# Optimization experiments

Hardware: AMD Instinct MI355X
Metric: run time of the kernel (lower is better)

## Reference

```python
import jax, jax.numpy as jnp
import numpy as np

N_NODES = 512
STATE_DIM = 32
MESSAGE_DIM = 32
H_MSG = 64
H_RO = 64
N_STEPS = 5


def setup_inputs() -> dict:
    key = jax.random.key(0)
    ks = jax.random.split(key, 20)
    s = 0.01  # torch init: normal(0, 0.01) weights, zero biases
    d, m = STATE_DIM, MESSAGE_DIM
    inp = {
        "J": jax.random.normal(ks[0], (N_NODES, N_NODES), jnp.float32),
        "b": jax.random.normal(ks[1], (N_NODES,), jnp.float32),
        # message-passing MLP
        "mp_W1": jax.random.normal(ks[2], (H_MSG, 2 * d + 3), jnp.float32) * s,
        "mp_b1": jnp.zeros((H_MSG,), jnp.float32),
        "mp_W2": jax.random.normal(ks[3], (H_MSG, H_MSG), jnp.float32) * s,
        "mp_b2": jnp.zeros((H_MSG,), jnp.float32),
        "mp_W3": jax.random.normal(ks[4], (m, H_MSG), jnp.float32) * s,
        "mp_b3": jnp.zeros((m,), jnp.float32),
        # GRU (input = state_dim + message_dim, hidden = state_dim); gate order r,z,n
        "gru_Wih": jax.random.normal(ks[5], (3 * d, d + m), jnp.float32) * 0.1,
        "gru_Whh": jax.random.normal(ks[6], (3 * d, d), jnp.float32) * 0.1,
        "gru_bih": jax.random.normal(ks[7], (3 * d,), jnp.float32) * 0.1,
        "gru_bhh": jax.random.normal(ks[8], (3 * d,), jnp.float32) * 0.1,
        # readout MLP
        "r_W1": jax.random.normal(ks[9], (H_RO, d), jnp.float32) * s,
        "r_b1": jnp.zeros((H_RO,), jnp.float32),
        "r_W2": jax.random.normal(ks[10], (H_RO, H_RO), jnp.float32) * s,
        "r_b2": jnp.zeros((H_RO,), jnp.float32),
        "r_W3": jax.random.normal(ks[11], (2, H_RO), jnp.float32) * s,
        "r_b3": jnp.zeros((2,), jnp.float32),
    }
    return inp


def reference(J, b, mp_W1, mp_b1, mp_W2, mp_b2, mp_W3, mp_b3,
              gru_Wih, gru_Whh, gru_bih, gru_bhh,
              r_W1, r_b1, r_W2, r_b2, r_W3, r_b3):
    n = J.shape[0]
    d = gru_Whh.shape[1]
    # split first message-layer weight by input segments to avoid building [n,n,2d+3]
    Wi, Wj = mp_W1[:, :d], mp_W1[:, d:2 * d]          # [H, d]
    wJ, wbi, wbj = mp_W1[:, 2 * d], mp_W1[:, 2 * d + 1], mp_W1[:, 2 * d + 2]  # [H]

    def step(h, _):
        # pre[i, j, :] = W1 @ cat(h_i, h_j, J_ij, b_i, b_j) + b1
        pre = ((h @ Wi.T)[:, None, :] + (h @ Wj.T)[None, :, :]
               + J[:, :, None] * wJ + b[:, None, None] * wbi
               + b[None, :, None] * wbj + mp_b1)          # [n, n, H]
        m1 = jax.nn.relu(pre)
        m2 = jax.nn.relu(m1 @ mp_W2.T + mp_b2)            # [n, n, H]
        msg = jax.nn.relu(m2 @ mp_W3.T + mp_b3)           # [n, n, M]
        msg_sum = msg.sum(axis=0)                         # sum over senders i -> [n, M]
        # GRU cell over all nodes (torch GRU, gate order r,z,n)
        x = jnp.concatenate([h, msg_sum], axis=-1)        # [n, d+M]
        gi = x @ gru_Wih.T + gru_bih                      # [n, 3d]
        gh = h @ gru_Whh.T + gru_bhh                      # [n, 3d]
        i_r, i_z, i_n = jnp.split(gi, 3, axis=-1)
        h_r, h_z, h_n = jnp.split(gh, 3, axis=-1)
        r = jax.nn.sigmoid(i_r + h_r)
        z = jax.nn.sigmoid(i_z + h_z)
        n_g = jnp.tanh(i_n + r * h_n)
        h_new = (1.0 - z) * n_g + z * h
        return h_new, None

    h0 = jnp.zeros((n, d), J.dtype)
    h, _ = jax.lax.scan(step, h0, None, length=N_STEPS)
    y = jax.nn.relu(h @ r_W1.T + r_b1)
    y = jax.nn.relu(y @ r_W2.T + r_b2)
    y = jax.nn.relu(y @ r_W3.T + r_b3)                    # [n, 2]
    return jax.nn.sigmoid(y)
```

## Files before the change

kernel.cpp:

```cpp
#include <hip/hip_runtime.h>
#include <math.h>

#define NN 512
#define SD 32
#define HM 64

typedef _Float16 f16x8 __attribute__((ext_vector_type(8)));
typedef float floatx4 __attribute__((ext_vector_type(4)));
typedef unsigned uintx4 __attribute__((ext_vector_type(4)));

#define OFF_HBS   0
#define OFF_M2L   73728
#define OFF_MSUM  92160
#define OFF_HPREV 93184
#define OFF_HS    93440
#define OFF_MSG   93696
#define OFF_GI    93952
#define OFF_GH    94720
#define LDS_TOTAL 95488

__device__ __forceinline__ float sigmoidf_(float x) {
    return 1.0f / (1.0f + __expf(-x));
}
__device__ __forceinline__ unsigned pkrtz(float a, float b) {
    unsigned r;
    asm("v_cvt_pkrtz_f16_f32 %0, %1, %2" : "=v"(r) : "v"(a), "v"(b));
    return r;
}
__device__ __forceinline__ unsigned pk_add(unsigned a, unsigned b) {
    unsigned r;
    asm("v_pk_add_f16 %0, %1, %2" : "=v"(r) : "v"(a), "v"(b));
    return r;
}
__device__ __forceinline__ unsigned pk_fma(unsigned a, unsigned b, unsigned c) {
    unsigned r;
    asm("v_pk_fma_f16 %0, %1, %2, %3" : "=v"(r) : "v"(a), "v"(b), "v"(c));
    return r;
}
__device__ __forceinline__ unsigned pk_relu(unsigned a) {
    unsigned r, z = 0u;
    asm("v_pk_max_f16 %0, %1, %2" : "=v"(r) : "v"(a), "v"(z));
    return r;
}

struct PParams {
    const float *J, *b, *mpW1, *mpb1, *mpW2, *mpW3, *Wih, *Whh, *rW1, *rW2;
    float *JT, *W1T, *WihT, *WhhT, *rW1T, *rW2T;
    unsigned *w2p, *w3p, *wjp, *hb0, *hjp0;
};

__global__ __launch_bounds__(256) void prep_kernel(PParams pp)
{
    __shared__ float tile[32][33];
    const int tid = threadIdx.x;
    const int b   = blockIdx.x;
    {
        int bx = b & 15, by = b >> 4;
        int tx = tid & 31, ty = tid >> 5;
        #pragma unroll
        for (int r = 0; r < 32; r += 8)
            tile[ty + r][tx] = pp.J[(by * 32 + ty + r) * NN + bx * 32 + tx];
        __syncthreads();
        #pragma unroll
        for (int r = 0; r < 32; r += 8)
            pp.JT[(bx * 32 + ty + r) * NN + by * 32 + tx] = tile[tx][ty + r];
    }
    if (b == 0 && tid < 64) {
        int l = tid, qq = l >> 4, cc = l & 15;
        for (int f = 0; f < 2; ++f)
            for (int t4 = 0; t4 < 4; ++t4) {
                const float* src = pp.mpW2 + (t4 * 16 + cc) * 64 + f * 32 + qq * 8;
                unsigned* dst = pp.w2p + ((f * 4 + t4) * 64 + l) * 4;
                for (int i = 0; i < 4; ++i) dst[i] = pkrtz(src[2 * i], src[2 * i + 1]);
            }
        for (int f = 0; f < 2; ++f)
            for (int t2 = 0; t2 < 2; ++t2) {
                const float* src = pp.mpW3 + (t2 * 16 + cc) * 64 + f * 32 + qq * 8;
                unsigned* dst = pp.w3p + ((f * 2 + t2) * 64 + l) * 4;
                for (int i = 0; i < 4; ++i) dst[i] = pkrtz(src[2 * i], src[2 * i + 1]);
            }
        for (int s = 0; s < 2; ++s) {
            unsigned* dst = pp.wjp + (s * 64 + l) * 4;
            for (int i = 0; i < 4; ++i) {
                int r0 = qq * 8 + 2 * i + s * 32;
                dst[i] = pkrtz(pp.mpW1[r0 * 67 + 64], pp.mpW1[(r0 + 1) * 67 + 64]);
            }
        }
    }
    if (b == 1)
        for (int n = tid; n < 64 * 67; n += 256) {
            int cc = n / 67, d = n % 67;
            pp.W1T[d * 64 + cc] = pp.mpW1[n];
        }
    if (b == 2)
        for (int n = tid; n < 96 * 64; n += 256)
            pp.WihT[(n & 63) * 96 + (n >> 6)] = pp.Wih[n];
    if (b == 3)
        for (int n = tid; n < 96 * 32; n += 256)
            pp.WhhT[(n & 31) * 96 + (n >> 5)] = pp.Whh[n];
    if (b == 4) {
        for (int n = tid; n < 64 * 32; n += 256)
            pp.rW1T[(n & 31) * 64 + (n >> 5)] = pp.rW1[n];
        for (int n = tid; n < 64 * 64; n += 256)
            pp.rW2T[(n & 63) * 64 + (n >> 6)] = pp.rW2[n];
    }
    if (b >= 16 && b < 144) {
        int jj = (b - 16) * 4 + (tid >> 6);
        int cc = tid & 63;
        float bj = pp.b[jj];
        float sj = bj * pp.mpW1[cc * 67 + 66] + pp.mpb1[cc];
        float si = bj * pp.mpW1[cc * 67 + 65];
        float sjp = __shfl(sj, cc ^ 1);
        float sip = __shfl(si, cc ^ 1);
        if (!(cc & 1)) {
            pp.hjp0[jj * 32 + (cc >> 1)] = pkrtz(sj, sjp);
            pp.hb0[jj * 32 + (cc >> 1)]  = pkrtz(si, sip);
        }
    }
}

struct SParams {
    const unsigned *hbR;  unsigned *hbW;
    const unsigned *hjR;  unsigned *hjW;
    const float *hR;      float *hW;
    const float *JT, *W1T, *WihT, *WhhT, *bih, *bhh, *mpb2, *mpb3, *b, *mpb1;
    const float *rW1T, *rW2T, *rW3, *rb1, *rb2, *rb3;
    const unsigned *w2p, *w3p, *wjp;
    float *out;
    int hzero, rdout;
};

__global__ __launch_bounds__(512, 1) void step_kernel(SParams s)
{
    extern __shared__ __align__(16) char smem[];
    char* hbS = smem + OFF_HBS;
    float (*msum)[32]   = (float(*)[32])(smem + OFF_MSUM);
    float (*hPrevS)[32] = (float(*)[32])(smem + OFF_HPREV);
    float (*hS)[32]     = (float(*)[32])(smem + OFF_HS);
    float (*msgS)[32]   = (float(*)[32])(smem + OFF_MSG);
    float (*giS)[96]    = (float(*)[96])(smem + OFF_GI);
    float (*ghS)[96]    = (float(*)[96])(smem + OFF_GH);

    const int tid  = threadIdx.x;
    const int lane = tid & 63;
    const int wave = tid >> 6;
    const int nsel = wave >> 2;
    const int nw   = wave & 3;
    const int j    = blockIdx.x * 2 + nsel;
    const int q    = lane >> 4;
    const int c    = lane & 15;
    char* m2Lw = smem + OFF_M2L + wave * 2304;

    {
        uintx4 cr[8];
        const uintx4* gp = (const uintx4*)s.hbR;
        #pragma unroll
        for (int k = 0; k < 8; ++k) cr[k] = gp[k * 512 + tid];
        #pragma unroll
        for (int k = 0; k < 8; ++k) {
            int row = k * 64 + (tid >> 3);
            *(uintx4*)(hbS + row * 144 + (tid & 7) * 16) = cr[k];
        }
    }
    if (tid < 64 && !s.hzero)
        hPrevS[tid >> 5][tid & 31] = s.hR[blockIdx.x * 64 + tid];
    __syncthreads();

    f16x8 Aw2[2][4], Aw3[2][2];
    #pragma unroll
    for (int f = 0; f < 2; ++f)
        #pragma unroll
        for (int t4 = 0; t4 < 4; ++t4)
            Aw2[f][t4] = __builtin_bit_cast(f16x8,
                ((const uintx4*)s.w2p)[(f * 4 + t4) * 64 + lane]);
    #pragma unroll
    for (int f = 0; f < 2; ++f)
        #pragma unroll
        for (int t2 = 0; t2 < 2; ++t2)
            Aw3[f][t2] = __builtin_bit_cast(f16x8,
                ((const uintx4*)s.w3p)[(f * 2 + t2) * 64 + lane]);
    uintx4 wja = ((const uintx4*)s.wjp)[lane];
    uintx4 wjb = ((const uintx4*)s.wjp)[64 + lane];
    uintx4 hja = ((const uintx4*)s.hjR)[j * 8 + q];
    uintx4 hjb = ((const uintx4*)s.hjR)[j * 8 + 4 + q];

    floatx4 b2i[4], b3i[2];
    #pragma unroll
    for (int t4 = 0; t4 < 4; ++t4)
        #pragma unroll
        for (int r = 0; r < 4; ++r) b2i[t4][r] = s.mpb2[t4 * 16 + q * 4 + r];
    #pragma unroll
    for (int t2 = 0; t2 < 2; ++t2)
        #pragma unroll
        for (int r = 0; r < 4; ++r) b3i[t2][r] = s.mpb3[t2 * 16 + q * 4 + r];

    const float jA = s.JT[j * NN + (8 * q + nw) * 16 + c];
    const float jB = s.JT[j * NN + (8 * q + 4 + nw) * 16 + c];

    float accf[2][4];
    #pragma unroll
    for (int t2 = 0; t2 < 2; ++t2)
        #pragma unroll
        for (int r = 0; r < 4; ++r) accf[t2][r] = 0.0f;

    auto edge_group = [&](int G, float Jv) {
        const char* rb = hbS + (G * 16 + c) * 144;
        uintx4 vlo = *(const uintx4*)(rb + q * 16);
        uintx4 vhi = *(const uintx4*)(rb + 64 + q * 16);
        const unsigned Jp = pkrtz(Jv, Jv);

        uintx4 a0u, a1u;
        #pragma unroll
        for (int i = 0; i < 4; ++i) {
            a0u[i] = pk_relu(pk_fma(Jp, wja[i], pk_add(vlo[i], hja[i])));
            a1u[i] = pk_relu(pk_fma(Jp, wjb[i], pk_add(vhi[i], hjb[i])));
        }
        f16x8 B0 = __builtin_bit_cast(f16x8, a0u);
        f16x8 B1 = __builtin_bit_cast(f16x8, a1u);

        floatx4 c1[4];
        #pragma unroll
        for (int t4 = 0; t4 < 4; ++t4) {
            c1[t4] = __builtin_amdgcn_mfma_f32_16x16x32_f16(Aw2[0][t4], B0, b2i[t4], 0, 0, 0);
            c1[t4] = __builtin_amdgcn_mfma_f32_16x16x32_f16(Aw2[1][t4], B1, c1[t4], 0, 0, 0);
        }
        #pragma unroll
        for (int t4 = 0; t4 < 4; ++t4) {
            unsigned p0 = pkrtz(fmaxf(c1[t4][0], 0.f), fmaxf(c1[t4][1], 0.f));
            unsigned p1 = pkrtz(fmaxf(c1[t4][2], 0.f), fmaxf(c1[t4][3], 0.f));
            *(uint2*)(m2Lw + c * 144 + t4 * 32 + q * 8) = make_uint2(p0, p1);
        }
        uintx4 rlo = *(const uintx4*)(m2Lw + c * 144 + q * 16);
        uintx4 rhi = *(const uintx4*)(m2Lw + c * 144 + 64 + q * 16);
        f16x8 B2lo = __builtin_bit_cast(f16x8, rlo);
        f16x8 B2hi = __builtin_bit_cast(f16x8, rhi);

        floatx4 c2[2];
        #pragma unroll
        for (int t2 = 0; t2 < 2; ++t2) {
            c2[t2] = __builtin_amdgcn_mfma_f32_16x16x32_f16(Aw3[0][t2], B2lo, b3i[t2], 0, 0, 0);
            c2[t2] = __builtin_amdgcn_mfma_f32_16x16x32_f16(Aw3[1][t2], B2hi, c2[t2], 0, 0, 0);
        }
        #pragma unroll
        for (int t2 = 0; t2 < 2; ++t2)
            #pragma unroll
            for (int r = 0; r < 4; ++r)
                accf[t2][r] += fmaxf(c2[t2][r], 0.0f);
    };

    #pragma unroll
    for (int k = 0; k < 4; ++k) {
        edge_group(8 * k + nw,     __shfl(jA, k * 16 + c));
        edge_group(8 * k + 4 + nw, __shfl(jB, k * 16 + c));
    }

    #pragma unroll
    for (int m = 1; m < 16; m <<= 1)
        #pragma unroll
        for (int t2 = 0; t2 < 2; ++t2)
            #pragma unroll
            for (int r = 0; r < 4; ++r)
                accf[t2][r] += __shfl_xor(accf[t2][r], m);
    if (c == 0) {
        #pragma unroll
        for (int t2 = 0; t2 < 2; ++t2)
            #pragma unroll
            for (int r = 0; r < 4; ++r)
                msum[wave][t2 * 16 + q * 4 + r] = accf[t2][r];
    }
    __syncthreads();

    if (tid < 64) {
        int node = tid >> 5, d = tid & 31;
        msgS[node][d] = msum[node * 4 + 0][d] + msum[node * 4 + 1][d] +
                        msum[node * 4 + 2][d] + msum[node * 4 + 3][d];
    }
    __syncthreads();

    if (tid < 192) {
        int node = tid / 96, r = tid % 96;
        float a  = s.bih[r];
        float bb = s.bhh[r];
        if (!s.hzero) {
            #pragma unroll
            for (int k = 0; k < 32; ++k) {
                float hv = hPrevS[node][k];
                a  = fmaf(hv, s.WihT[k * 96 + r], a);
                bb = fmaf(hv, s.WhhT[k * 96 + r], bb);
            }
        }
        #pragma unroll
        for (int k = 0; k < 32; ++k)
            a = fmaf(msgS[node][k], s.WihT[(32 + k) * 96 + r], a);
        giS[node][r] = a; ghS[node][r] = bb;
    }
    __syncthreads();

    if (tid < 64) {
        int node = tid >> 5, d = tid & 31;
        float r  = sigmoidf_(giS[node][d] + ghS[node][d]);
        float z  = sigmoidf_(giS[node][32 + d] + ghS[node][32 + d]);
        float ng = tanhf(giS[node][64 + d] + r * ghS[node][64 + d]);
        float hold = s.hzero ? 0.0f : hPrevS[node][d];
        float hv = (1.0f - z) * ng + z * hold;
        hS[node][d] = hv;
        s.hW[blockIdx.x * 64 + tid] = hv;
    }
    __syncthreads();

    if (!s.rdout) {
        if (tid < 128) {
            int node = tid >> 6, cc = tid & 63;
            int jj = blockIdx.x * 2 + node;
            float bj = s.b[jj];
            float si = bj * s.W1T[65 * 64 + cc];
            float sj = bj * s.W1T[66 * 64 + cc] + s.mpb1[cc];
            #pragma unroll
            for (int d = 0; d < 32; ++d) {
                float hv = hS[node][d];
                si = fmaf(hv, s.W1T[d * 64 + cc], si);
                sj = fmaf(hv, s.W1T[(32 + d) * 64 + cc], sj);
            }
            float sip = __shfl(si, lane ^ 1);
            float sjp = __shfl(sj, lane ^ 1);
            if (!(cc & 1)) {
                s.hbW[jj * 32 + (cc >> 1)] = pkrtz(si, sip);
                s.hjW[jj * 32 + (cc >> 1)] = pkrtz(sj, sjp);
            }
        }
    } else {
        if (wave < 2) {
            int node = wave;
            int jj = blockIdx.x * 2 + node;
            float y1 = s.rb1[lane];
            #pragma unroll
            for (int k = 0; k < 32; ++k)
                y1 = fmaf(hS[node][k], s.rW1T[k * 64 + lane], y1);
            y1 = fmaxf(y1, 0.0f);
            float y2 = s.rb2[lane];
            #pragma unroll
            for (int k = 0; k < 64; ++k)
                y2 = fmaf(__shfl(y1, k), s.rW2T[k * 64 + lane], y2);
            y2 = fmaxf(y2, 0.0f);
            float y3 = (lane < 2) ? s.rb3[lane] : 0.0f;
            #pragma unroll
            for (int k = 0; k < 64; ++k) {
                float v = __shfl(y2, k);
                if (lane < 2) y3 = fmaf(v, s.rW3[lane * 64 + k], y3);
            }
            if (lane < 2) s.out[jj * 2 + lane] = sigmoidf_(y3);
        }
    }
}

extern "C" void kernel_launch(void* const* d_in, const int* in_sizes, int n_in,
                              void* d_out, int out_size, void* d_ws, size_t ws_size,
                              hipStream_t stream)
{
    float* ws = (float*)d_ws;

    const float* J    = (const float*)d_in[0];
    const float* b    = (const float*)d_in[1];
    const float* mpW1 = (const float*)d_in[2];
    const float* mpb1 = (const float*)d_in[3];
    const float* mpW2 = (const float*)d_in[4];
    const float* mpb2 = (const float*)d_in[5];
    const float* mpW3 = (const float*)d_in[6];
    const float* mpb3 = (const float*)d_in[7];
    const float* Wih  = (const float*)d_in[8];
    const float* Whh  = (const float*)d_in[9];
    const float* bih  = (const float*)d_in[10];
    const float* bhh  = (const float*)d_in[11];
    const float* rW1  = (const float*)d_in[12];
    const float* rb1  = (const float*)d_in[13];
    const float* rW2  = (const float*)d_in[14];
    const float* rb2  = (const float*)d_in[15];
    const float* rW3  = (const float*)d_in[16];
    const float* rb3  = (const float*)d_in[17];

    float*    JT   = ws;
    float*    W1T  = ws + 262144;
    float*    WihT = ws + 266432;
    float*    WhhT = ws + 272576;
    float*    rW1T = ws + 275648;
    float*    rW2T = ws + 277696;
    unsigned* w2p  = (unsigned*)(ws + 281792);
    unsigned* w3p  = (unsigned*)(ws + 283840);
    unsigned* wjp  = (unsigned*)(ws + 284864);
    unsigned* hb0  = (unsigned*)(ws + 285376);
    unsigned* hb1  = (unsigned*)(ws + 301760);
    unsigned* hj0  = (unsigned*)(ws + 318144);
    unsigned* hj1  = (unsigned*)(ws + 334528);
    float*    h0   = ws + 350912;
    float*    h1   = ws + 367296;

    PParams pp;
    pp.J = J; pp.b = b; pp.mpW1 = mpW1; pp.mpb1 = mpb1; pp.mpW2 = mpW2;
    pp.mpW3 = mpW3; pp.Wih = Wih; pp.Whh = Whh; pp.rW1 = rW1; pp.rW2 = rW2;
    pp.JT = JT; pp.W1T = W1T; pp.WihT = WihT; pp.WhhT = WhhT;
    pp.rW1T = rW1T; pp.rW2T = rW2T;
    pp.w2p = w2p; pp.w3p = w3p; pp.wjp = wjp; pp.hb0 = hb0; pp.hjp0 = hj0;

    (void)hipFuncSetAttribute((const void*)step_kernel,
                              hipFuncAttributeMaxDynamicSharedMemorySize, LDS_TOTAL);

    prep_kernel<<<dim3(256), dim3(256), 0, stream>>>(pp);

    SParams s;
    s.JT = JT; s.W1T = W1T; s.WihT = WihT; s.WhhT = WhhT;
    s.bih = bih; s.bhh = bhh; s.mpb2 = mpb2; s.mpb3 = mpb3; s.b = b; s.mpb1 = mpb1;
    s.rW1T = rW1T; s.rW2T = rW2T; s.rW3 = rW3; s.rb1 = rb1; s.rb2 = rb2; s.rb3 = rb3;
    s.w2p = w2p; s.w3p = w3p; s.wjp = wjp;
    s.out = (float*)d_out;

    for (int t = 0; t < 5; ++t) {
        s.hbR = (t & 1) ? hb1 : hb0;
        s.hbW = (t & 1) ? hb0 : hb1;
        s.hjR = (t & 1) ? hj1 : hj0;
        s.hjW = (t & 1) ? hj0 : hj1;
        s.hR  = (t & 1) ? h0 : h1;
        s.hW  = (t & 1) ? h1 : h0;
        s.hzero = (t == 0);
        s.rdout = (t == 4);
        step_kernel<<<dim3(256), dim3(512), LDS_TOTAL, stream>>>(s);
    }
}
```

Measured before the change: 150.7 us.

## Fuse prep and five step launches into one persistent kernel with grid barriers

New measurement: 330.2 us. +119.1%, slower.

```diff
diff --git a/kernel.cpp b/kernel.cpp
--- a/kernel.cpp
+++ b/kernel.cpp
@@ -4,6 +4,7 @@
 #define NN 512
 #define SD 32
 #define HM 64
+#define NB 256
 
 typedef _Float16 f16x8 __attribute__((ext_vector_type(8)));
 typedef float floatx4 __attribute__((ext_vector_type(4)));
@@ -17,7 +18,11 @@
 #define OFF_MSG   93696
 #define OFF_GI    93952
 #define OFF_GH    94720
-#define LDS_TOTAL 95488
+#define OFF_HJ    95488
+#define OFF_W1T   95744
+#define OFF_WIH   113168
+#define OFF_WHH   138000
+#define LDS_TOTAL 150416
 
 __device__ __forceinline__ float sigmoidf_(float x) {
     return 1.0f / (1.0f + __expf(-x));
@@ -43,96 +48,45 @@
     return r;
 }
 
-struct PParams {
-    const float *J, *b, *mpW1, *mpb1, *mpW2, *mpW3, *Wih, *Whh, *rW1, *rW2;
-    float *JT, *W1T, *WihT, *WhhT, *rW1T, *rW2T;
-    unsigned *w2p, *w3p, *wjp, *hb0, *hjp0;
+__device__ __forceinline__ void grid_bar(unsigned long long* pk, unsigned target_gen)
+{
+    __syncthreads();
+    if (threadIdx.x == 0) {
+        unsigned long long old =
+            __hip_atomic_fetch_add(pk, 1ull, __ATOMIC_RELAXED, __HIP_MEMORY_SCOPE_AGENT);
+        if ((unsigned)(old & 0xffffffffull) == (unsigned)(NB - 1))
+            __hip_atomic_store(pk, ((unsigned long long)target_gen) << 32,
+                               __ATOMIC_RELAXED, __HIP_MEMORY_SCOPE_AGENT);
+        while ((unsigned)(__hip_atomic_load(pk, __ATOMIC_RELAXED,
+                                            __HIP_MEMORY_SCOPE_AGENT) >> 32) < target_gen)
+            __builtin_amdgcn_s_sleep(2);
+        (void)__hip_atomic_load(pk, __ATOMIC_ACQUIRE, __HIP_MEMORY_SCOPE_AGENT);
+    }
+    __syncthreads();
+}
+
+struct FParams {
+    const float *J, *b, *mpW1, *mpb1, *mpW2, *mpb2, *mpW3, *mpb3;
+    const float *Wih, *Whh, *bih, *bhh;
+    const float *rW1, *rb1, *rW2, *rb2, *rW3, *rb3;
+    unsigned *hbg;
+    unsigned long long *bar;
+    float *out;
 };
 
-__global__ __launch_bounds__(256) void prep_kernel(PParams pp)
-{
-    __shared__ float tile[32][33];
-    const int tid = threadIdx.x;
-    const int b   = blockIdx.x;
-    {
-        int bx = b & 15, by = b >> 4;
-        int tx = tid & 31, ty = tid >> 5;
-        #pragma unroll
-        for (int r = 0; r < 32; r += 8)
-            tile[ty + r][tx] = pp.J[(by * 32 + ty + r) * NN + bx * 32 + tx];
-        __syncthreads();
-        #pragma unroll
-        for (int r = 0; r < 32; r += 8)
-            pp.JT[(bx * 32 + ty + r) * NN + by * 32 + tx] = tile[tx][ty + r];
-    }
-    if (b == 0 && tid < 64) {
-        int l = tid, qq = l >> 4, cc = l & 15;
-        for (int f = 0; f < 2; ++f)
-            for (int t4 = 0; t4 < 4; ++t4) {
-                const float* src = pp.mpW2 + (t4 * 16 + cc) * 64 + f * 32 + qq * 8;
-                unsigned* dst = pp.w2p + ((f * 4 + t4) * 64 + l) * 4;
-                for (int i = 0; i < 4; ++i) dst[i] = pkrtz(src[2 * i], src[2 * i + 1]);
-            }
-        for (int f = 0; f < 2; ++f)
-            for (int t2 = 0; t2 < 2; ++t2) {
-                const float* src = pp.mpW3 + (t2 * 16 + cc) * 64 + f * 32 + qq * 8;
-                unsigned* dst = pp.w3p + ((f * 2 + t2) * 64 + l) * 4;
-                for (int i = 0; i < 4; ++i) dst[i] = pkrtz(src[2 * i], src[2 * i + 1]);
-            }
-        for (int s = 0; s < 2; ++s) {
-            unsigned* dst = pp.wjp + (s * 64 + l) * 4;
-            for (int i = 0; i < 4; ++i) {
-                int r0 = qq * 8 + 2 * i + s * 32;
-                dst[i] = pkrtz(pp.mpW1[r0 * 67 + 64], pp.mpW1[(r0 + 1) * 67 + 64]);
-            }
-        }
-    }
-    if (b == 1)
-        for (int n = tid; n < 64 * 67; n += 256) {
-            int cc = n / 67, d = n % 67;
-            pp.W1T[d * 64 + cc] = pp.mpW1[n];
-        }
-    if (b == 2)
-        for (int n = tid; n < 96 * 64; n += 256)
-            pp.WihT[(n & 63) * 96 + (n >> 6)] = pp.Wih[n];
-    if (b == 3)
-        for (int n = tid; n < 96 * 32; n += 256)
-            pp.WhhT[(n & 31) * 96 + (n >> 5)] = pp.Whh[n];
-    if (b == 4) {
-        for (int n = tid; n < 64 * 32; n += 256)
-            pp.rW1T[(n & 31) * 64 + (n >> 5)] = pp.rW1[n];
-        for (int n = tid; n < 64 * 64; n += 256)
-            pp.rW2T[(n & 63) * 64 + (n >> 6)] = pp.rW2[n];
-    }
-    if (b >= 16 && b < 144) {
-        int jj = (b - 16) * 4 + (tid >> 6);
-        int cc = tid & 63;
-        float bj = pp.b[jj];
-        float sj = bj * pp.mpW1[cc * 67 + 66] + pp.mpb1[cc];
-        float si = bj * pp.mpW1[cc * 67 + 65];
-        float sjp = __shfl(sj, cc ^ 1);
-        float sip = __shfl(si, cc ^ 1);
-        if (!(cc & 1)) {
-            pp.hjp0[jj * 32 + (cc >> 1)] = pkrtz(sj, sjp);
-            pp.hb0[jj * 32 + (cc >> 1)]  = pkrtz(si, sip);
-        }
-    }
-}
-
-struct SParams {
-    const unsigned *hbR;  unsigned *hbW;
-    const unsigned *hjR;  unsigned *hjW;
-    const float *hR;      float *hW;
-    const float *JT, *W1T, *WihT, *WhhT, *bih, *bhh, *mpb2, *mpb3, *b, *mpb1;
-    const float *rW1T, *rW2T, *rW3, *rb1, *rb2, *rb3;
-    const unsigned *w2p, *w3p, *wjp;
-    float *out;
-    int hzero, rdout;
-};
-
-__global__ __launch_bounds__(512, 1) void step_kernel(SParams s)
+__global__ __launch_bounds__(512, 1) void fused3_kernel(FParams p)
 {
     extern __shared__ __align__(16) char smem[];
+    const int tid  = threadIdx.x;
+    const int bid  = blockIdx.x;
+    const int lane = tid & 63;
+    const int wave = tid >> 6;
+    const int nsel = wave >> 2;
+    const int nw   = wave & 3;
+    const int j    = bid * 2 + nsel;
+    const int q    = lane >> 4;
+    const int c    = lane & 15;
+
     char* hbS = smem + OFF_HBS;
     float (*msum)[32]   = (float(*)[32])(smem + OFF_MSUM);
     float (*hPrevS)[32] = (float(*)[32])(smem + OFF_HPREV);
@@ -140,215 +94,276 @@
     float (*msgS)[32]   = (float(*)[32])(smem + OFF_MSG);
     float (*giS)[96]    = (float(*)[96])(smem + OFF_GI);
     float (*ghS)[96]    = (float(*)[96])(smem + OFF_GH);
-
-    const int tid  = threadIdx.x;
-    const int lane = tid & 63;
-    const int wave = tid >> 6;
-    const int nsel = wave >> 2;
-    const int nw   = wave & 3;
-    const int j    = blockIdx.x * 2 + nsel;
-    const int q    = lane >> 4;
-    const int c    = lane & 15;
-    char* m2Lw = smem + OFF_M2L + wave * 2304;
-
-    {
-        uintx4 cr[8];
-        const uintx4* gp = (const uintx4*)s.hbR;
-        #pragma unroll
-        for (int k = 0; k < 8; ++k) cr[k] = gp[k * 512 + tid];
-        #pragma unroll
-        for (int k = 0; k < 8; ++k) {
-            int row = k * 64 + (tid >> 3);
-            *(uintx4*)(hbS + row * 144 + (tid & 7) * 16) = cr[k];
-        }
+    char*  hjL  = smem + OFF_HJ;
+    float* w1tL = (float*)(smem + OFF_W1T);
+    float* wihL = (float*)(smem + OFF_WIH);
+    float* whhL = (float*)(smem + OFF_WHH);
+    char*  m2Lw = smem + OFF_M2L + wave * 2304;
+
+    for (int n = tid; n < 64 * 67; n += 512) {
+        int cc = n / 67, d = n % 67;
+        w1tL[d * 65 + cc] = p.mpW1[n];
     }
-    if (tid < 64 && !s.hzero)
-        hPrevS[tid >> 5][tid & 31] = s.hR[blockIdx.x * 64 + tid];
-    __syncthreads();
+    for (int n = tid; n < 96 * 64; n += 512)
+        wihL[(n & 63) * 97 + (n >> 6)] = p.Wih[n];
+    for (int n = tid; n < 96 * 32; n += 512)
+        whhL[(n & 31) * 97 + (n >> 5)] = p.Whh[n];
 
     f16x8 Aw2[2][4], Aw3[2][2];
     #pragma unroll
     for (int f = 0; f < 2; ++f)
         #pragma unroll
-        for (int t4 = 0; t4 < 4; ++t4)
-            Aw2[f][t4] = __builtin_bit_cast(f16x8,
-                ((const uintx4*)s.w2p)[(f * 4 + t4) * 64 + lane]);
+        for (int t4 = 0; t4 < 4; ++t4) {
+            const float* src = p.mpW2 + (t4 * 16 + c) * 64 + f * 32 + q * 8;
+            floatx4 s0 = *(const floatx4*)(src);
+            floatx4 s1 = *(const floatx4*)(src + 4);
+            uintx4 u;
+            u[0] = pkrtz(s0[0], s0[1]); u[1] = pkrtz(s0[2], s0[3]);
+            u[2] = pkrtz(s1[0], s1[1]); u[3] = pkrtz(s1[2], s1[3]);
+            Aw2[f][t4] = __builtin_bit_cast(f16x8, u);
+        }
     #pragma unroll
     for (int f = 0; f < 2; ++f)
         #pragma unroll
-        for (int t2 = 0; t2 < 2; ++t2)
-            Aw3[f][t2] = __builtin_bit_cast(f16x8,
-                ((const uintx4*)s.w3p)[(f * 2 + t2) * 64 + lane]);
-    uintx4 wja = ((const uintx4*)s.wjp)[lane];
-    uintx4 wjb = ((const uintx4*)s.wjp)[64 + lane];
-    uintx4 hja = ((const uintx4*)s.hjR)[j * 8 + q];
-    uintx4 hjb = ((const uintx4*)s.hjR)[j * 8 + 4 + q];
-
+        for (int t2 = 0; t2 < 2; ++t2) {
+            const float* src = p.mpW3 + (t2 * 16 + c) * 64 + f * 32 + q * 8;
+            floatx4 s0 = *(const floatx4*)(src);
+            floatx4 s1 = *(const floatx4*)(src + 4);
+            uintx4 u;
+            u[0] = pkrtz(s0[0], s0[1]); u[1] = pkrtz(s0[2], s0[3]);
+            u[2] = pkrtz(s1[0], s1[1]); u[3] = pkrtz(s1[2], s1[3]);
+            Aw3[f][t2] = __builtin_bit_cast(f16x8, u);
+        }
+    uintx4 wja, wjb;
+    #pragma unroll
+    for (int i = 0; i < 4; ++i) {
+        int r0 = q * 8 + 2 * i;
+        wja[i] = pkrtz(p.mpW1[r0 * 67 + 64], p.mpW1[(r0 + 1) * 67 + 64]);
+        int r1 = r0 + 32;
+        wjb[i] = pkrtz(p.mpW1[r1 * 67 + 64], p.mpW1[(r1 + 1) * 67 + 64]);
+    }
     floatx4 b2i[4], b3i[2];
     #pragma unroll
     for (int t4 = 0; t4 < 4; ++t4)
         #pragma unroll
-        for (int r = 0; r < 4; ++r) b2i[t4][r] = s.mpb2[t4 * 16 + q * 4 + r];
+        for (int r = 0; r < 4; ++r) b2i[t4][r] = p.mpb2[t4 * 16 + q * 4 + r];
     #pragma unroll
     for (int t2 = 0; t2 < 2; ++t2)
         #pragma unroll
-        for (int r = 0; r < 4; ++r) b3i[t2][r] = s.mpb3[t2 * 16 + q * 4 + r];
-
-    const float jA = s.JT[j * NN + (8 * q + nw) * 16 + c];
-    const float jB = s.JT[j * NN + (8 * q + 4 + nw) * 16 + c];
-
-    float accf[2][4];
-    #pragma unroll
-    for (int t2 = 0; t2 < 2; ++t2)
-        #pragma unroll
-        for (int r = 0; r < 4; ++r) accf[t2][r] = 0.0f;
-
-    auto edge_group = [&](int G, float Jv) {
-        const char* rb = hbS + (G * 16 + c) * 144;
-        uintx4 vlo = *(const uintx4*)(rb + q * 16);
-        uintx4 vhi = *(const uintx4*)(rb + 64 + q * 16);
-        const unsigned Jp = pkrtz(Jv, Jv);
-
-        uintx4 a0u, a1u;
-        #pragma unroll
-        for (int i = 0; i < 4; ++i) {
-            a0u[i] = pk_relu(pk_fma(Jp, wja[i], pk_add(vlo[i], hja[i])));
-            a1u[i] = pk_relu(pk_fma(Jp, wjb[i], pk_add(vhi[i], hjb[i])));
-        }
-        f16x8 B0 = __builtin_bit_cast(f16x8, a0u);
-        f16x8 B1 = __builtin_bit_cast(f16x8, a1u);
-
-        floatx4 c1[4];
-        #pragma unroll
-        for (int t4 = 0; t4 < 4; ++t4) {
-            c1[t4] = __builtin_amdgcn_mfma_f32_16x16x32_f16(Aw2[0][t4], B0, b2i[t4], 0, 0, 0);
-            c1[t4] = __builtin_amdgcn_mfma_f32_16x16x32_f16(Aw2[1][t4], B1, c1[t4], 0, 0, 0);
-        }
-        #pragma unroll
-        for (int t4 = 0; t4 < 4; ++t4) {
-            unsigned p0 = pkrtz(fmaxf(c1[t4][0], 0.f), fmaxf(c1[t4][1], 0.f));
-            unsigned p1 = pkrtz(fmaxf(c1[t4][2], 0.f), fmaxf(c1[t4][3], 0.f));
-            *(uint2*)(m2Lw + c * 144 + t4 * 32 + q * 8) = make_uint2(p0, p1);
-        }
-        uintx4 rlo = *(const uintx4*)(m2Lw + c * 144 + q * 16);
-        uintx4 rhi = *(const uintx4*)(m2Lw + c * 144 + 64 + q * 16);
-        f16x8 B2lo = __builtin_bit_cast(f16x8, rlo);
-        f16x8 B2hi = __builtin_bit_cast(f16x8, rhi);
-
-        floatx4 c2[2];
-        #pragma unroll
-        for (int t2 = 0; t2 < 2; ++t2) {
-            c2[t2] = __builtin_amdgcn_mfma_f32_16x16x32_f16(Aw3[0][t2], B2lo, b3i[t2], 0, 0, 0);
-            c2[t2] = __builtin_amdgcn_mfma_f32_16x16x32_f16(Aw3[1][t2], B2hi, c2[t2], 0, 0, 0);
-        }
+        for (int r = 0; r < 4; ++r) b3i[t2][r] = p.mpb3[t2 * 16 + q * 4 + r];
+
+    const float jA = p.J[((8 * q + nw) * 16 + c) * NN + j];
+    const float jB = p.J[((8 * q + 4 + nw) * 16 + c) * NN + j];
+
+    __syncthreads();
+
+    if (tid < 128) {
+        int node = tid >> 6, cc = tid & 63;
+        int jj = bid * 2 + node;
+        float bj = p.b[jj];
+        float si = bj * w1tL[65 * 65 + cc];
+        float sj = bj * w1tL[66 * 65 + cc] + p.mpb1[cc];
+        float sip = __shfl(si, lane ^ 1);
+        float sjp = __shfl(sj, lane ^ 1);
+        if (!(cc & 1)) {
+            __hip_atomic_store(&p.hbg[jj * 32 + (cc >> 1)], pkrtz(si, sip),
+                               __ATOMIC_RELAXED, __HIP_MEMORY_SCOPE_AGENT);
+            *(unsigned*)(hjL + node * 128 + (cc >> 1) * 4) = pkrtz(sj, sjp);
+        }
+    }
+    grid_bar(p.bar, 1);
+
+    #pragma unroll 1
+    for (int t = 0; t < 5; ++t) {
+        {
+            const unsigned long long* gq =
+                (const unsigned long long*)(p.hbg + t * 16384);
+            uintx4 cr[8];
+            #pragma unroll
+            for (int k = 0; k < 8; ++k) {
+                unsigned long long lo = __hip_atomic_load(gq + (k * 512 + tid) * 2,
+                    __ATOMIC_RELAXED, __HIP_MEMORY_SCOPE_AGENT);
+                unsigned long long hi = __hip_atomic_load(gq + (k * 512 + tid) * 2 + 1,
+                    __ATOMIC_RELAXED, __HIP_MEMORY_SCOPE_AGENT);
+                cr[k][0] = (unsigned)lo; cr[k][1] = (unsigned)(lo >> 32);
+                cr[k][2] = (unsigned)hi; cr[k][3] = (unsigned)(hi >> 32);
+            }
+            #pragma unroll
+            for (int k = 0; k < 8; ++k) {
+                int row = k * 64 + (tid >> 3);
+                *(uintx4*)(hbS + row * 144 + (tid & 7) * 16) = cr[k];
+            }
+        }
+        uintx4 hja = *(const uintx4*)(hjL + nsel * 128 + q * 16);
+        uintx4 hjb = *(const uintx4*)(hjL + nsel * 128 + 64 + q * 16);
+        __syncthreads();
+
+        float accf[2][4];
         #pragma unroll
         for (int t2 = 0; t2 < 2; ++t2)
             #pragma unroll
-            for (int r = 0; r < 4; ++r)
-                accf[t2][r] += fmaxf(c2[t2][r], 0.0f);
-    };
-
-    #pragma unroll
-    for (int k = 0; k < 4; ++k) {
-        edge_group(8 * k + nw,     __shfl(jA, k * 16 + c));
-        edge_group(8 * k + 4 + nw, __shfl(jB, k * 16 + c));
-    }
-
-    #pragma unroll
-    for (int m = 1; m < 16; m <<= 1)
-        #pragma unroll
-        for (int t2 = 0; t2 < 2; ++t2)
-            #pragma unroll
-            for (int r = 0; r < 4; ++r)
-                accf[t2][r] += __shfl_xor(accf[t2][r], m);
-    if (c == 0) {
-        #pragma unroll
-        for (int t2 = 0; t2 < 2; ++t2)
-            #pragma unroll
-            for (int r = 0; r < 4; ++r)
-                msum[wave][t2 * 16 + q * 4 + r] = accf[t2][r];
-    }
-    __syncthreads();
-
-    if (tid < 64) {
-        int node = tid >> 5, d = tid & 31;
-        msgS[node][d] = msum[node * 4 + 0][d] + msum[node * 4 + 1][d] +
-                        msum[node * 4 + 2][d] + msum[node * 4 + 3][d];
-    }
-    __syncthreads();
-
-    if (tid < 192) {
-        int node = tid / 96, r = tid % 96;
-        float a  = s.bih[r];
-        float bb = s.bhh[r];
-        if (!s.hzero) {
-            #pragma unroll
-            for (int k = 0; k < 32; ++k) {
-                float hv = hPrevS[node][k];
-                a  = fmaf(hv, s.WihT[k * 96 + r], a);
-                bb = fmaf(hv, s.WhhT[k * 96 + r], bb);
-            }
-        }
-        #pragma unroll
-        for (int k = 0; k < 32; ++k)
-            a = fmaf(msgS[node][k], s.WihT[(32 + k) * 96 + r], a);
-        giS[node][r] = a; ghS[node][r] = bb;
-    }
-    __syncthreads();
-
-    if (tid < 64) {
-        int node = tid >> 5, d = tid & 31;
-        float r  = sigmoidf_(giS[node][d] + ghS[node][d]);
-        float z  = sigmoidf_(giS[node][32 + d] + ghS[node][32 + d]);
-        float ng = tanhf(giS[node][64 + d] + r * ghS[node][64 + d]);
-        float hold = s.hzero ? 0.0f : hPrevS[node][d];
-        float hv = (1.0f - z) * ng + z * hold;
-        hS[node][d] = hv;
-        s.hW[blockIdx.x * 64 + tid] = hv;
-    }
-    __syncthreads();
-
-    if (!s.rdout) {
-        if (tid < 128) {
-            int node = tid >> 6, cc = tid & 63;
-            int jj = blockIdx.x * 2 + node;
-            float bj = s.b[jj];
-            float si = bj * s.W1T[65 * 64 + cc];
-            float sj = bj * s.W1T[66 * 64 + cc] + s.mpb1[cc];
-            #pragma unroll
-            for (int d = 0; d < 32; ++d) {
-                float hv = hS[node][d];
-                si = fmaf(hv, s.W1T[d * 64 + cc], si);
-                sj = fmaf(hv, s.W1T[(32 + d) * 64 + cc], sj);
-            }
-            float sip = __shfl(si, lane ^ 1);
-            float sjp = __shfl(sj, lane ^ 1);
-            if (!(cc & 1)) {
-                s.hbW[jj * 32 + (cc >> 1)] = pkrtz(si, sip);
-                s.hjW[jj * 32 + (cc >> 1)] = pkrtz(sj, sjp);
-            }
-        }
-    } else {
-        if (wave < 2) {
-            int node = wave;
-            int jj = blockIdx.x * 2 + node;
-            float y1 = s.rb1[lane];
+            for (int r = 0; r < 4; ++r) accf[t2][r] = 0.0f;
+
+        auto edge_group = [&](int G, float Jv) {
+            const char* rb = hbS + (G * 16 + c) * 144;
+            uintx4 vlo = *(const uintx4*)(rb + q * 16);
+            uintx4 vhi = *(const uintx4*)(rb + 64 + q * 16);
+            const unsigned Jp = pkrtz(Jv, Jv);
+
+            uintx4 a0u, a1u;
+            #pragma unroll
+            for (int i = 0; i < 4; ++i) {
+                a0u[i] = pk_relu(pk_fma(Jp, wja[i], pk_add(vlo[i], hja[i])));
+                a1u[i] = pk_relu(pk_fma(Jp, wjb[i], pk_add(vhi[i], hjb[i])));
+            }
+            f16x8 B0 = __builtin_bit_cast(f16x8, a0u);
+            f16x8 B1 = __builtin_bit_cast(f16x8, a1u);
+
+            floatx4 c1[4];
+            #pragma unroll
+            for (int t4 = 0; t4 < 4; ++t4) {
+                c1[t4] = __builtin_amdgcn_mfma_f32_16x16x32_f16(Aw2[0][t4], B0, b2i[t4], 0, 0, 0);
+                c1[t4] = __builtin_amdgcn_mfma_f32_16x16x32_f16(Aw2[1][t4], B1, c1[t4], 0, 0, 0);
+            }
+            #pragma unroll
+            for (int t4 = 0; t4 < 4; ++t4) {
+                unsigned p0 = pkrtz(fmaxf(c1[t4][0], 0.f), fmaxf(c1[t4][1], 0.f));
+                unsigned p1 = pkrtz(fmaxf(c1[t4][2], 0.f), fmaxf(c1[t4][3], 0.f));
+                *(uint2*)(m2Lw + c * 144 + t4 * 32 + q * 8) = make_uint2(p0, p1);
+            }
+            uintx4 rlo = *(const uintx4*)(m2Lw + c * 144 + q * 16);
+            uintx4 rhi = *(const uintx4*)(m2Lw + c * 144 + 64 + q * 16);
+            f16x8 B2lo = __builtin_bit_cast(f16x8, rlo);
+            f16x8 B2hi = __builtin_bit_cast(f16x8, rhi);
+
+            floatx4 c2[2];
+            #pragma unroll
+            for (int t2 = 0; t2 < 2; ++t2) {
+                c2[t2] = __builtin_amdgcn_mfma_f32_16x16x32_f16(Aw3[0][t2], B2lo, b3i[t2], 0, 0, 0);
+                c2[t2] = __builtin_amdgcn_mfma_f32_16x16x32_f16(Aw3[1][t2], B2hi, c2[t2], 0, 0, 0);
+            }
+            #pragma unroll
+            for (int t2 = 0; t2 < 2; ++t2)
+                #pragma unroll
+                for (int r = 0; r < 4; ++r)
+                    accf[t2][r] += fmaxf(c2[t2][r], 0.0f);
+        };
+
+        #pragma unroll
+        for (int k = 0; k < 4; ++k) {
+            edge_group(8 * k + nw,     __shfl(jA, k * 16 + c));
+            edge_group(8 * k + 4 + nw, __shfl(jB, k * 16 + c));
+        }
+
+        #pragma unroll
+        for (int m = 1; m < 16; m <<= 1)
+            #pragma unroll
+            for (int t2 = 0; t2 < 2; ++t2)
+                #pragma unroll
+                for (int r = 0; r < 4; ++r)
+                    accf[t2][r] += __shfl_xor(accf[t2][r], m);
+        if (c == 0) {
+            #pragma unroll
+            for (int t2 = 0; t2 < 2; ++t2)
+                #pragma unroll
+                for (int r = 0; r < 4; ++r)
+                    msum[wave][t2 * 16 + q * 4 + r] = accf[t2][r];
+        }
+        __syncthreads();
+
+        if (tid < 64) {
+            int node = tid >> 5, d = tid & 31;
+            msgS[node][d] = msum[node * 4 + 0][d] + msum[node * 4 + 1][d] +
+                            msum[node * 4 + 2][d] + msum[node * 4 + 3][d];
+        }
+        __syncthreads();
+
+        if (tid < 192) {
+            int node = tid / 96, r = tid % 96;
+            float a  = p.bih[r];
+            float bb = p.bhh[r];
+            if (t != 0) {
+                #pragma unroll
+                for (int k = 0; k < 32; ++k) {
+                    float hv = hPrevS[node][k];
+                    a  = fmaf(hv, wihL[k * 97 + r], a);
+                    bb = fmaf(hv, whhL[k * 97 + r], bb);
+                }
+            }
             #pragma unroll
             for (int k = 0; k < 32; ++k)
-                y1 = fmaf(hS[node][k], s.rW1T[k * 64 + lane], y1);
-            y1 = fmaxf(y1, 0.0f);
-            float y2 = s.rb2[lane];
-            #pragma unroll
-            for (int k = 0; k < 64; ++k)
-                y2 = fmaf(__shfl(y1, k), s.rW2T[k * 64 + lane], y2);
-            y2 = fmaxf(y2, 0.0f);
-            float y3 = (lane < 2) ? s.rb3[lane] : 0.0f;
-            #pragma unroll
-            for (int k = 0; k < 64; ++k) {
-                float v = __shfl(y2, k);
-                if (lane < 2) y3 = fmaf(v, s.rW3[lane * 64 + k], y3);
-            }
-            if (lane < 2) s.out[jj * 2 + lane] = sigmoidf_(y3);
+                a = fmaf(msgS[node][k], wihL[(32 + k) * 97 + r], a);
+            giS[node][r] = a; ghS[node][r] = bb;
+        }
+        __syncthreads();
+
+        if (tid < 64) {
+            int node = tid >> 5, d = tid & 31;
+            float r  = sigmoidf_(giS[node][d] + ghS[node][d]);
+            float z  = sigmoidf_(giS[node][32 + d] + ghS[node][32 + d]);
+            float ng = tanhf(giS[node][64 + d] + r * ghS[node][64 + d]);
+            float hold = (t == 0) ? 0.0f : hPrevS[node][d];
+            float hv = (1.0f - z) * ng + z * hold;
+            hS[node][d] = hv;
+            hPrevS[node][d] = hv;
+        }
+        __syncthreads();
+
+        if (t < 4) {
+            if (tid < 128) {
+                int node = tid >> 6, cc = tid & 63;
+                int jj = bid * 2 + node;
+                float bj = p.b[jj];
+                float si = bj * w1tL[65 * 65 + cc];
+                float sj = bj * w1tL[66 * 65 + cc] + p.mpb1[cc];
+                #pragma unroll
+                for (int d = 0; d < 32; ++d) {
+                    float hv = hS[node][d];
+                    si = fmaf(hv, w1tL[d * 65 + cc], si);
+                    sj = fmaf(hv, w1tL[(32 + d) * 65 + cc], sj);
+                }
+                float sip = __shfl(si, lane ^ 1);
+                float sjp = __shfl(sj, lane ^ 1);
+                if (!(cc & 1)) {
+                    __hip_atomic_store(&p.hbg[(t + 1) * 16384 + jj * 32 + (cc >> 1)],
+                                       pkrtz(si, sip),
+                                       __ATOMIC_RELAXED, __HIP_MEMORY_SCOPE_AGENT);
+                    *(unsigned*)(hjL + node * 128 + (cc >> 1) * 4) = pkrtz(sj, sjp);
+                }
+            }
+            grid_bar(p.bar, (unsigned)(t + 2));
+        } else {
+            if (wave < 2) {
+                int node = wave;
+                int jj = bid * 2 + node;
+                float y1 = p.rb1[lane];
+                const floatx4* w1p = (const floatx4*)(p.rW1 + lane * 32);
+                #pragma unroll
+                for (int kk = 0; kk < 8; ++kk) {
+                    floatx4 v = w1p[kk];
+                    #pragma unroll
+                    for (int i = 0; i < 4; ++i)
+                        y1 = fmaf(hS[node][kk * 4 + i], v[i], y1);
+                }
+                y1 = fmaxf(y1, 0.0f);
+                float y2 = p.rb2[lane];
+                const floatx4* w2p = (const floatx4*)(p.rW2 + lane * 64);
+                #pragma unroll
+                for (int kk = 0; kk < 16; ++kk) {
+                    floatx4 v = w2p[kk];
+                    #pragma unroll
+                    for (int i = 0; i < 4; ++i)
+                        y2 = fmaf(__shfl(y1, kk * 4 + i), v[i], y2);
+                }
+                y2 = fmaxf(y2, 0.0f);
+                float y3 = (lane < 2) ? p.rb3[lane] : 0.0f;
+                #pragma unroll
+                for (int k = 0; k < 64; ++k) {
+                    float v = __shfl(y2, k);
+                    if (lane < 2) y3 = fmaf(v, p.rW3[lane * 64 + k], y3);
+                }
+                if (lane < 2) p.out[jj * 2 + lane] = sigmoidf_(y3);
+            }
         }
     }
 }
@@ -378,50 +393,21 @@
     const float* rW3  = (const float*)d_in[16];
     const float* rb3  = (const float*)d_in[17];
 
-    float*    JT   = ws;
-    float*    W1T  = ws + 262144;
-    float*    WihT = ws + 266432;
-    float*    WhhT = ws + 272576;
-    float*    rW1T = ws + 275648;
-    float*    rW2T = ws + 277696;
-    unsigned* w2p  = (unsigned*)(ws + 281792);
-    unsigned* w3p  = (unsigned*)(ws + 283840);
-    unsigned* wjp  = (unsigned*)(ws + 284864);
-    unsigned* hb0  = (unsigned*)(ws + 285376);
-    unsigned* hb1  = (unsigned*)(ws + 301760);
-    unsigned* hj0  = (unsigned*)(ws + 318144);
-    unsigned* hj1  = (unsigned*)(ws + 334528);
-    float*    h0   = ws + 350912;
-    float*    h1   = ws + 367296;
-
-    PParams pp;
-    pp.J = J; pp.b = b; pp.mpW1 = mpW1; pp.mpb1 = mpb1; pp.mpW2 = mpW2;
-    pp.mpW3 = mpW3; pp.Wih = Wih; pp.Whh = Whh; pp.rW1 = rW1; pp.rW2 = rW2;
-    pp.JT = JT; pp.W1T = W1T; pp.WihT = WihT; pp.WhhT = WhhT;
-    pp.rW1T = rW1T; pp.rW2T = rW2T;
-    pp.w2p = w2p; pp.w3p = w3p; pp.wjp = wjp; pp.hb0 = hb0; pp.hjp0 = hj0;
-
-    (void)hipFuncSetAttribute((const void*)step_kernel,
+    unsigned* hbg = (unsigned*)(ws + 2097152);
+    unsigned long long* bar = (unsigned long long*)(ws + 2097152 + 5 * 16384);
+
+    (void)hipFuncSetAttribute((const void*)fused3_kernel,
                               hipFuncAttributeMaxDynamicSharedMemorySize, LDS_TOTAL);
 
-    prep_kernel<<<dim3(256), dim3(256), 0, stream>>>(pp);
-
-    SParams s;
-    s.JT = JT; s.W1T = W1T; s.WihT = WihT; s.WhhT = WhhT;
-    s.bih = bih; s.bhh = bhh; s.mpb2 = mpb2; s.mpb3 = mpb3; s.b = b; s.mpb1 = mpb1;
-    s.rW1T = rW1T; s.rW2T = rW2T; s.rW3 = rW3; s.rb1 = rb1; s.rb2 = rb2; s.rb3 = rb3;
-    s.w2p = w2p; s.w3p = w3p; s.wjp = wjp;
-    s.out = (float*)d_out;
-
-    for (int t = 0; t < 5; ++t) {
-        s.hbR = (t & 1) ? hb1 : hb0;
-        s.hbW = (t & 1) ? hb0 : hb1;
-        s.hjR = (t & 1) ? hj1 : hj0;
-        s.hjW = (t & 1) ? hj0 : hj1;
-        s.hR  = (t & 1) ? h0 : h1;
-        s.hW  = (t & 1) ? h1 : h0;
-        s.hzero = (t == 0);
-        s.rdout = (t == 4);
-        step_kernel<<<dim3(256), dim3(512), LDS_TOTAL, stream>>>(s);
-    }
-}
+    FParams fp;
+    fp.J = J; fp.b = b; fp.mpW1 = mpW1; fp.mpb1 = mpb1; fp.mpW2 = mpW2;
+    fp.mpb2 = mpb2; fp.mpW3 = mpW3; fp.mpb3 = mpb3;
+    fp.Wih = Wih; fp.Whh = Whh; fp.bih = bih; fp.bhh = bhh;
+    fp.rW1 = rW1; fp.rb1 = rb1; fp.rW2 = rW2; fp.rb2 = rb2; fp.rW3 = rW3; fp.rb3 = rb3;
+    fp.hbg = hbg; fp.bar = bar;
+    fp.out = (float*)d_out;
+
+    (void)hipMemsetAsync((void*)bar, 0, 128, stream);
+
+    fused3_kernel<<<dim3(NB), dim3(512), LDS_TOTAL, stream>>>(fp);
+}
```
